# Kernel tuning notes

Hardware: AMD Instinct MI355X
Metric: run time of the kernel (lower is better)

## Reference

```python
import jax, jax.numpy as jnp
import numpy as np

HIDDEN = 1024
HEADS = 16
HEAD_DIM = HIDDEN // HEADS  # 64
MLP_HIDDEN = int(HIDDEN * 4.0)  # 4096
B, L = 2, 2048
EPS_LN = 1e-6
EPS_RMS = 1e-6


def setup_inputs() -> dict:
    key = jax.random.key(0)
    ks = jax.random.split(key, 12)
    s = 0.02
    return {
        "x": jax.random.normal(ks[0], (B, L, HIDDEN), jnp.float32),
        "vec": jax.random.normal(ks[1], (B, HIDDEN), jnp.float32),
        "pe": jax.random.normal(ks[2], (1, 1, L, HEAD_DIM // 2, 2, 2), jnp.float32),
        "w_mod": jax.random.normal(ks[3], (HIDDEN, 3 * HIDDEN), jnp.float32) * s,
        "b_mod": jnp.zeros((3 * HIDDEN,), jnp.float32),
        "w1": jax.random.normal(ks[4], (HIDDEN, 3 * HIDDEN + MLP_HIDDEN), jnp.float32) * s,
        "b1": jnp.zeros((3 * HIDDEN + MLP_HIDDEN,), jnp.float32),
        "w_mlp": jax.random.normal(ks[5], (MLP_HIDDEN, HIDDEN), jnp.float32) * s,
        "b_mlp": jnp.zeros((HIDDEN,), jnp.float32),
        "w2": jax.random.normal(ks[6], (2 * HIDDEN, HIDDEN), jnp.float32) * s,
        "b2": jnp.zeros((HIDDEN,), jnp.float32),
        "q_scale": jnp.ones((HEAD_DIM,), jnp.float32),
        "k_scale": jnp.ones((HEAD_DIM,), jnp.float32),
    }


def _layernorm(x, eps=EPS_LN):
    m = jnp.mean(x, axis=-1, keepdims=True)
    v = jnp.mean(jnp.square(x - m), axis=-1, keepdims=True)
    return (x - m) * jax.lax.rsqrt(v + eps)


def _rmsnorm(x, scale, eps=EPS_RMS):
    rrms = jax.lax.rsqrt(jnp.mean(jnp.square(x), axis=-1, keepdims=True) + eps)
    return x * rrms * scale


def _apply_rope(t, pe):
    # t: [B,H,L,D]; pe: [1,1,L,D//2,2,2]
    t_ = t.reshape(*t.shape[:-1], -1, 1, 2)  # [B,H,L,D//2,1,2]
    out = pe[..., 0] * t_[..., 0] + pe[..., 1] * t_[..., 1]  # [B,H,L,D//2,2]
    return out.reshape(t.shape)


def reference(x, vec, pe, w_mod, b_mod, w1, b1, w_mlp, b_mlp, w2, b2, q_scale, k_scale):
    # adaLN modulation: silu(vec) -> Dense(3*dim) -> shift, scale, gate
    mod = (jax.nn.silu(vec) @ w_mod + b_mod)[:, None, :]  # [B,1,3H]
    shift, scale, gate = jnp.split(mod, 3, axis=-1)
    x_mod = (1.0 + scale) * _layernorm(x) + shift
    # fused QKV + MLP projection
    h = x_mod @ w1 + b1  # [B,L,3H+MH]
    qkv, mlp = h[..., : 3 * HIDDEN], h[..., 3 * HIDDEN :]
    qkv = qkv.reshape(x.shape[0], x.shape[1], 3, HEADS, HEAD_DIM)
    qkv = jnp.transpose(qkv, (2, 0, 3, 1, 4))  # [3,B,H,L,D]
    q, k, v = qkv[0], qkv[1], qkv[2]
    # QK-RMSNorm per head-dim
    q = _rmsnorm(q, q_scale)
    k = _rmsnorm(k, k_scale)
    # RoPE
    q = _apply_rope(q, pe)
    k = _apply_rope(k, pe)
    # attention
    scores = jnp.einsum("bhqd,bhkd->bhqk", q, k) * (HEAD_DIM ** -0.5)
    probs = jax.nn.softmax(scores, axis=-1)
    attn = jnp.einsum("bhqk,bhkd->bhqd", probs, v)
    attn = jnp.transpose(attn, (0, 2, 1, 3)).reshape(x.shape[0], x.shape[1], HIDDEN)
    # mlp branch (Dense with tanh activation per source) + fused output proj
    mlp_out = jnp.tanh(mlp @ w_mlp + b_mlp)
    out = jnp.concatenate([attn, mlp_out], axis=-1) @ w2 + b2
    return x + gate * out
```

## Files before the change

### kernel.cpp

```cpp
#include <hip/hip_runtime.h>
#include <stdint.h>


#define HID  1024
#define NH   16
#define HD   64
#define MLP  4096
#define D1   7168
#define DQKV 3072
#define DCAT 2048
#define BB   2
#define LL   2048
#define TOK  4096

typedef __attribute__((ext_vector_type(8))) short    bf16x8;
typedef __attribute__((ext_vector_type(4))) float    f32x4;
typedef __attribute__((ext_vector_type(4))) unsigned int u32x4;

__device__ __forceinline__ float b2f(unsigned short u) {
    unsigned int v = ((unsigned int)u) << 16;
    float f; __builtin_memcpy(&f, &v, 4); return f;
}
__device__ __forceinline__ unsigned short f2b(float f) {
    unsigned int v; __builtin_memcpy(&v, &f, 4);
    unsigned int r = (v + 0x7FFFu + ((v >> 16) & 1u)) >> 16;
    return (unsigned short)r;
}
__device__ __forceinline__ unsigned int pkbf2(float a, float b) {
    unsigned int ua, ub;
    __builtin_memcpy(&ua, &a, 4); __builtin_memcpy(&ub, &b, 4);
    return ((ua + 0x8000u) >> 16) | ((ub + 0x8000u) & 0xFFFF0000u);
}
__device__ __forceinline__ void gl_lds16(const unsigned short* g, unsigned short* l) {
    __builtin_amdgcn_global_load_lds(
        (const __attribute__((address_space(1))) unsigned int*)(g),
        (__attribute__((address_space(3))) unsigned int*)(l), 16, 0, 0);
}

__global__ void k_transpose_cvt(const float* __restrict__ in,
                                unsigned short* __restrict__ out, int R, int C) {
    __shared__ float tile[32][33];
    int bx = blockIdx.x, by = blockIdx.y;
    int tx = threadIdx.x, ty = threadIdx.y;
    #pragma unroll
    for (int i = 0; i < 4; i++) {
        int r = by * 32 + ty + i * 8;
        int c = bx * 32 + tx;
        tile[ty + i * 8][tx] = in[(size_t)r * C + c];
    }
    __syncthreads();
    #pragma unroll
    for (int i = 0; i < 4; i++) {
        int ro = bx * 32 + ty + i * 8;
        int co = by * 32 + tx;
        out[(size_t)ro * R + co] = f2b(tile[tx][ty + i * 8]);
    }
}

__global__ void k_mod(const float* __restrict__ vec,
                      const float* __restrict__ w_mod,
                      const float* __restrict__ b_mod,
                      float* __restrict__ mod) {
    __shared__ float sv[HID];
    __shared__ float red[8][32];
    int b = blockIdx.y, t = threadIdx.x;
    for (int j = t; j < HID; j += 256) {
        float v = vec[b * HID + j];
        sv[j] = v / (1.0f + __expf(-v));
    }
    __syncthreads();
    int n0 = blockIdx.x * 32;
    int on = t & 31, ks = t >> 5;
    float acc = 0.f;
    const float* wp = w_mod + (size_t)(ks * 128) * 3072 + n0 + on;
    #pragma unroll 4
    for (int k = 0; k < 128; k++) acc += sv[ks * 128 + k] * wp[(size_t)k * 3072];
    red[ks][on] = acc;
    __syncthreads();
    if (t < 32) {
        float s = 0.f;
        #pragma unroll
        for (int i = 0; i < 8; i++) s += red[i][t];
        mod[b * 3072 + n0 + t] = s + b_mod[n0 + t];
    }
}

__global__ void k_lnmod(const float* __restrict__ x,
                        const float* __restrict__ mod,
                        unsigned short* __restrict__ xmod) {
    int tok = blockIdx.x;
    int t = threadIdx.x;
    int b = tok >> 11;
    float4 v4 = *(const float4*)(x + (size_t)tok * HID + t * 4);
    float v0 = v4.x, v1 = v4.y, v2 = v4.z, v3 = v4.w;
    float s  = v0 + v1 + v2 + v3;
    float sq = v0*v0 + v1*v1 + v2*v2 + v3*v3;
    for (int off = 1; off < 64; off <<= 1) {
        s  += __shfl_xor(s,  off);
        sq += __shfl_xor(sq, off);
    }
    __shared__ float ls[4], lq[4];
    int w = t >> 6;
    if ((t & 63) == 0) { ls[w] = s; lq[w] = sq; }
    __syncthreads();
    s  = ls[0] + ls[1] + ls[2] + ls[3];
    sq = lq[0] + lq[1] + lq[2] + lq[3];
    float mean = s * (1.0f / HID);
    float var  = sq * (1.0f / HID) - mean * mean;
    float rstd = rsqrtf(var + 1e-6f);
    const float* mb = mod + b * 3072;
    float y[4] = {v0, v1, v2, v3};
    unsigned short r[4];
    #pragma unroll
    for (int j = 0; j < 4; j++) {
        int col = t * 4 + j;
        float nval = (y[j] - mean) * rstd;
        r[j] = f2b((1.0f + mb[1024 + col]) * nval + mb[col]);
    }
    unsigned int o0 = (unsigned int)r[0] | ((unsigned int)r[1] << 16);
    unsigned int o1 = (unsigned int)r[2] | ((unsigned int)r[3] << 16);
    *(uint2*)(xmod + (size_t)tok * HID + t * 4) = make_uint2(o0, o1);
}

template<int EPI>
__global__ __launch_bounds__(256) void k_gemm(
    const unsigned short* __restrict__ A, int lda,
    const unsigned short* __restrict__ Bt, int ldb,
    const float* __restrict__ bias,
    unsigned short* __restrict__ C, float* __restrict__ Cf, int ldc,
    int K,
    const float* __restrict__ xin,
    const float* __restrict__ mod) {
    __shared__ alignas(16) unsigned short As[128 * 64];
    __shared__ alignas(16) unsigned short Bs[128 * 64];
    int t = threadIdx.x;
    int bm = blockIdx.x, bn = blockIdx.y;
    int lane = t & 63, wave = t >> 6;
    int wm = (wave >> 1) * 64, wn = (wave & 1) * 64;
    int ln = lane & 15, kq = lane >> 4;
    int ln7 = ln & 7;

    f32x4 acc[4][4];
    #pragma unroll
    for (int i = 0; i < 4; i++)
        #pragma unroll
        for (int j = 0; j < 4; j++) acc[i][j] = {0.f, 0.f, 0.f, 0.f};

    int sr  = t >> 3;
    int scg = (t & 7) ^ (sr & 7);
    const unsigned short* Ab = A  + (size_t)(bm * 128) * lda;
    const unsigned short* Bb = Bt + (size_t)(bn * 128) * ldb;

    int ksplit = K / gridDim.z;
    int kbeg = blockIdx.z * ksplit, kend = kbeg + ksplit;

    for (int k0 = kbeg; k0 < kend; k0 += 64) {
        __syncthreads();
        #pragma unroll
        for (int c = 0; c < 4; c++) {
            gl_lds16(Ab + (size_t)(c * 32 + sr) * lda + k0 + scg * 8, &As[c * 2048 + t * 8]);
            gl_lds16(Bb + (size_t)(c * 32 + sr) * ldb + k0 + scg * 8, &Bs[c * 2048 + t * 8]);
        }
        __syncthreads();
        #pragma unroll
        for (int ks = 0; ks < 2; ks++) {
            int slot = ((ks * 4 + kq) ^ ln7) * 8;
            bf16x8 af[4], bfr[4];
            #pragma unroll
            for (int i = 0; i < 4; i++)
                af[i] = *(const bf16x8*)(&As[(wm + i * 16 + ln) * 64 + slot]);
            #pragma unroll
            for (int j = 0; j < 4; j++)
                bfr[j] = *(const bf16x8*)(&Bs[(wn + j * 16 + ln) * 64 + slot]);
            #pragma unroll
            for (int i = 0; i < 4; i++)
                #pragma unroll
                for (int j = 0; j < 4; j++)
                    acc[i][j] = __builtin_amdgcn_mfma_f32_16x16x32_bf16(af[i], bfr[j], acc[i][j], 0, 0, 0);
        }
    }

    #pragma unroll
    for (int i = 0; i < 4; i++) {
        #pragma unroll
        for (int j = 0; j < 4; j++) {
            int col = bn * 128 + wn + j * 16 + ln;
            float bv = (EPI == 3) ? 0.f : bias[col];
            #pragma unroll
            for (int r = 0; r < 4; r++) {
                int row = bm * 128 + wm + i * 16 + kq * 4 + r;
                float v = acc[i][j][r] + bv;
                if (EPI == 0) {
                    C[(size_t)row * ldc + col] = f2b(v);
                } else if (EPI == 1) {
                    C[(size_t)row * ldc + col] = f2b(tanhf(v));
                } else if (EPI == 2) {
                    int b = row >> 11;
                    Cf[(size_t)row * ldc + col] =
                        xin[(size_t)row * HID + col] + mod[b * 3072 + 2048 + col] * v;
                } else {
                    Cf[((size_t)blockIdx.z * TOK + row) * ldc + col] = v;
                }
            }
        }
    }
}

#define KD   1024
#define NT16 16

#define STAGE_A2(BUF, H, KO) do { \
    const unsigned short* s_ = Ab + (size_t)((H) * 128 + sr) * KD + (KO) + scg8; \
    gl_lds16(s_,            &As[BUF][H][t * 8]); \
    gl_lds16(s_ + 64 * KD,  &As[BUF][H][4096 + t * 8]); \
  } while (0)

#define STAGE_B2(BUF, H, KO) do { \
    const unsigned short* s_ = Bb + (size_t)((H) * 128 + sr) * KD + (KO) + scg8; \
    gl_lds16(s_,            &Bs[BUF][H][t * 8]); \
    gl_lds16(s_ + 64 * KD,  &Bs[BUF][H][4096 + t * 8]); \
  } while (0)

#define LDA_H(DST, BUF, MH) do { \
    _Pragma("unroll") \
    for (int i_ = 0; i_ < 4; i_++) { \
      const unsigned short* ap_ = &As[BUF][wmh][(MH) * 4096 + i_ * 1024 + lnx64]; \
      DST[i_][0] = *(const bf16x8*)(ap_ + sA0); \
      DST[i_][1] = *(const bf16x8*)(ap_ + sA1); \
    } \
  } while (0)

#define LDB_H(DST, BUF, NH) do { \
    _Pragma("unroll") \
    for (int j_ = 0; j_ < 2; j_++) { \
      const unsigned short* bp_ = &Bs[BUF][wnh][bro + (NH) * 2048 + j_ * 1024 + lnx64]; \
      DST[j_][0] = *(const bf16x8*)(bp_ + sA0); \
      DST[j_][1] = *(const bf16x8*)(bp_ + sA1); \
    } \
  } while (0)

#define MMQ(AF, BF, IG0, JG0) do { \
    __builtin_amdgcn_s_setprio(1); \
    _Pragma("unroll") \
    for (int ks_ = 0; ks_ < 2; ks_++) \
      _Pragma("unroll") \
      for (int i_ = 0; i_ < 4; i_++) \
        _Pragma("unroll") \
        for (int j_ = 0; j_ < 2; j_++) \
          acc[(IG0) + i_][(JG0) + j_] = __builtin_amdgcn_mfma_f32_16x16x32_bf16( \
              AF[i_][ks_], BF[j_][ks_], acc[(IG0) + i_][(JG0) + j_], 0, 0, 0); \
    __builtin_amdgcn_s_setprio(0); \
  } while (0)

__global__ __launch_bounds__(512, 2) void k_gemm256(
    const unsigned short* __restrict__ A,
    const unsigned short* __restrict__ Bt,
    const float* __restrict__ bias,
    unsigned short* __restrict__ C) {
    __shared__ alignas(16) unsigned short As[2][2][128 * 64];
    __shared__ alignas(16) unsigned short Bs[2][2][128 * 64];

    int wg  = blockIdx.x;
    int cpx = gridDim.x >> 3;
    int swz = (wg & 7) * cpx + (wg >> 3);
    int bm = swz & 15;
    int bn = swz >> 4;

    int t = threadIdx.x;
    int lane = t & 63, wid = t >> 6;
    int wmh = wid >> 2;
    int wnq = wid & 3;
    int wnh = wnq >> 1;
    int bro = (wnq & 1) * 4096;
    int ln = lane & 15, kq = lane >> 4, ln7 = lane & 7;
    int lnx64 = ln * 64;
    int sA0 = ((0 + kq) ^ ln7) * 8;
    int sA1 = ((4 + kq) ^ ln7) * 8;

    int sr   = t >> 3;
    int scg8 = (((t & 7) ^ (sr & 7))) * 8;

    const unsigned short* Ab = A  + (size_t)(bm * 256) * KD;
    const unsigned short* Bb = Bt + (size_t)(bn * 256) * KD;

    f32x4 acc[8][4];
    #pragma unroll
    for (int i = 0; i < 8; i++)
        #pragma unroll
        for (int j = 0; j < 4; j++) acc[i][j] = {0.f, 0.f, 0.f, 0.f};

    STAGE_A2(0, 0, 0);  STAGE_A2(0, 1, 0);
    STAGE_B2(0, 0, 0);  STAGE_B2(0, 1, 0);
    STAGE_A2(1, 0, 64); STAGE_A2(1, 1, 64);
    asm volatile("s_waitcnt vmcnt(4)" ::: "memory");
    __builtin_amdgcn_sched_barrier(0);
    __builtin_amdgcn_s_barrier();

    bf16x8 afA[4][2], afB[4][2], bf0[2][2], bf1[2][2];

    for (int tau = 0; tau < NT16; ++tau) {
        const int q  = tau & 1;
        const int k0 = tau << 6;
        LDA_H(afA, q, 0);
        LDB_H(bf0, q, 0);
        if (tau + 1 < NT16) STAGE_B2(q ^ 1, 0, k0 + 64);
        __builtin_amdgcn_s_barrier();
        asm volatile("s_waitcnt lgkmcnt(0)" ::: "memory");
        __builtin_amdgcn_sched_barrier(0);
        MMQ(afA, bf0, 0, 0);
        __builtin_amdgcn_s_barrier();
        LDA_H(afB, q, 1);
        LDB_H(bf1, q, 1);
        if (tau + 1 < NT16) STAGE_B2(q ^ 1, 1, k0 + 64);
        __builtin_amdgcn_s_barrier();
        asm volatile("s_waitcnt lgkmcnt(0)" ::: "memory");
        __builtin_amdgcn_sched_barrier(0);
        MMQ(afA, bf1, 0, 2);
        __builtin_amdgcn_s_barrier();
        if (tau + 2 < NT16) STAGE_A2(q, 0, k0 + 128);
        MMQ(afB, bf1, 4, 2);
        __builtin_amdgcn_s_barrier();
        if (tau + 2 < NT16) STAGE_A2(q, 1, k0 + 128);
        MMQ(afB, bf0, 4, 0);
        if (tau + 2 < NT16) {
            asm volatile("s_waitcnt vmcnt(4)" ::: "memory");
        } else if (tau + 1 < NT16) {
            asm volatile("s_waitcnt vmcnt(0)" ::: "memory");
        }
        __builtin_amdgcn_sched_barrier(0);
        __builtin_amdgcn_s_barrier();
    }

    #pragma unroll
    for (int jg = 0; jg < 4; jg++) {
        int col = bn * 256 + wnq * 64 + jg * 16 + ln;
        float bv = bias[col];
        #pragma unroll
        for (int ig = 0; ig < 8; ig++) {
            int row = bm * 256 + wmh * 128 + ig * 16 + kq * 4;
            #pragma unroll
            for (int r = 0; r < 4; r++)
                C[(size_t)(row + r) * D1 + col] = f2b(acc[ig][jg][r] + bv);
        }
    }
}

__global__ __launch_bounds__(256) void k_red1(const float* __restrict__ part,
                                              const float* __restrict__ bias,
                                              unsigned short* __restrict__ cat) {
    int idx = blockIdx.x * 256 + threadIdx.x;
    int row = idx >> 8;
    int c4  = (idx & 255) * 4;
    float4 p0 = *(const float4*)(part + (size_t)row * HID + c4);
    float4 p1 = *(const float4*)(part + ((size_t)TOK + row) * HID + c4);
    float4 bv = *(const float4*)(bias + c4);
    float a0 = tanhf(p0.x + p1.x + bv.x);
    float a1 = tanhf(p0.y + p1.y + bv.y);
    float a2 = tanhf(p0.z + p1.z + bv.z);
    float a3 = tanhf(p0.w + p1.w + bv.w);
    *(uint2*)(&cat[(size_t)row * DCAT + HID + c4]) =
        make_uint2(pkbf2(a0, a1), pkbf2(a2, a3));
}

__global__ __launch_bounds__(256) void k_red2(const float* __restrict__ part,
                                              const float* __restrict__ bias,
                                              const float* __restrict__ x,
                                              const float* __restrict__ mod,
                                              float* __restrict__ out) {
    int idx = blockIdx.x * 256 + threadIdx.x;
    int row = idx >> 8;
    int c4  = (idx & 255) * 4;
    int b = row >> 11;
    float4 p0 = *(const float4*)(part + (size_t)row * HID + c4);
    float4 p1 = *(const float4*)(part + ((size_t)TOK + row) * HID + c4);
    float4 bv = *(const float4*)(bias + c4);
    float4 gv = *(const float4*)(mod + b * 3072 + 2048 + c4);
    float4 xv = *(const float4*)(x + (size_t)row * HID + c4);
    float4 o;
    o.x = xv.x + gv.x * (p0.x + p1.x + bv.x);
    o.y = xv.y + gv.y * (p0.y + p1.y + bv.y);
    o.z = xv.z + gv.z * (p0.z + p1.z + bv.z);
    o.w = xv.w + gv.w * (p0.w + p1.w + bv.w);
    *(float4*)(out + (size_t)row * HID + c4) = o;
}

__global__ void k_qkrope(unsigned short* __restrict__ h,
                         const float* __restrict__ pe,
                         const float* __restrict__ q_scale,
                         const float* __restrict__ k_scale) {
    int tok = blockIdx.x;
    int l = tok & (LL - 1);
    int t = threadIdx.x;
    int lane = t & 63, wave = t >> 6;
    int hh = wave * 4 + (lane >> 4);
    int d0 = (lane & 15) * 4;
    unsigned short* row = h + (size_t)tok * D1;
    int i0 = d0 >> 1;
    const float* peb = pe + ((size_t)l * 32 + i0) * 4;
    float4 e0 = *(const float4*)(peb);
    float4 e1 = *(const float4*)(peb + 4);
    #pragma unroll
    for (int qk = 0; qk < 2; qk++) {
        unsigned short* p = row + qk * HID + hh * HD + d0;
        const float* sc = (qk == 0 ? q_scale : k_scale) + d0;
        uint2 qv = *(const uint2*)p;
        float v0 = b2f((unsigned short)(qv.x & 0xFFFF)), v1 = b2f((unsigned short)(qv.x >> 16));
        float v2 = b2f((unsigned short)(qv.y & 0xFFFF)), v3 = b2f((unsigned short)(qv.y >> 16));
        float ssq = v0*v0 + v1*v1 + v2*v2 + v3*v3;
        ssq += __shfl_xor(ssq, 1, 16);
        ssq += __shfl_xor(ssq, 2, 16);
        ssq += __shfl_xor(ssq, 4, 16);
        ssq += __shfl_xor(ssq, 8, 16);
        float rr = rsqrtf(ssq * (1.0f / HD) + 1e-6f);
        if (qk == 0) rr *= 0.18033688011112042f;
        v0 *= rr * sc[0];
        v1 *= rr * sc[1];
        v2 *= rr * sc[2];
        v3 *= rr * sc[3];
        float o0 = e0.x*v0 + e0.y*v1;
        float o1 = e0.z*v0 + e0.w*v1;
        float o2 = e1.x*v2 + e1.y*v3;
        float o3 = e1.z*v2 + e1.w*v3;
        *(uint2*)p = make_uint2(pkbf2(o0, o1), pkbf2(o2, o3));
    }
}

#define KT 64
#define LDP 72
__global__ __launch_bounds__(256) void k_attn(const unsigned short* __restrict__ h,
                                              unsigned short* __restrict__ cat) {
    __shared__ unsigned short Ks[KT * LDP];
    __shared__ unsigned short Vt[HD * LDP];
    __shared__ unsigned short Ps[4 * 16 * LDP];
    int t = threadIdx.x;
    int bx = blockIdx.x;
    int bh = blockIdx.y;
    int b = bh >> 4, hh = bh & 15;
    int lane = t & 63, w = t >> 6;
    int ln = lane & 15, quad = lane >> 4;
    const unsigned short* hb = h + (size_t)b * LL * D1;

    bf16x8 qf[2];
    {
        const unsigned short* qbase = hb + (size_t)(bx * 64 + w * 16) * D1 + hh * HD;
        #pragma unroll
        for (int ks = 0; ks < 2; ks++)
            qf[ks] = *(const bf16x8*)(qbase + (size_t)ln * D1 + ks * 32 + quad * 8);
    }

    f32x4 O[4];
    #pragma unroll
    for (int vn = 0; vn < 4; vn++) O[vn] = {0.f, 0.f, 0.f, 0.f};
    float m_ = -1e30f, l_ = 0.f;

    unsigned short* Psw = Ps + w * 16 * LDP;

    int skey = t >> 2, sdc = (t & 3) * 16;
    int p2 = (t & 31) * 2, db = (t >> 5) * 8;

    for (int kb = 0; kb < LL / KT; kb++) {
        __syncthreads();
        {
            const unsigned short* kbase = hb + (size_t)(kb * KT) * D1 + HID + hh * HD;
            u32x4 ka = *(const u32x4*)(kbase + (size_t)skey * D1 + sdc);
            u32x4 kc = *(const u32x4*)(kbase + (size_t)skey * D1 + sdc + 8);
            *(u32x4*)(&Ks[skey * LDP + sdc]) = ka;
            *(u32x4*)(&Ks[skey * LDP + sdc + 8]) = kc;
            const unsigned short* vbase = hb + (size_t)(kb * KT) * D1 + 2 * HID + hh * HD;
            u32x4 va = *(const u32x4*)(vbase + (size_t)p2 * D1 + db);
            u32x4 vb = *(const u32x4*)(vbase + (size_t)(p2 + 1) * D1 + db);
            #pragma unroll
            for (int j = 0; j < 8; j++) {
                unsigned int lo = (j & 1) ? (va[j >> 1] >> 16) : (va[j >> 1] & 0xFFFFu);
                unsigned int hi = (j & 1) ? (vb[j >> 1] >> 16) : (vb[j >> 1] & 0xFFFFu);
                *(unsigned int*)(&Vt[(db + j) * LDP + p2]) = lo | (hi << 16);
            }
        }
        __syncthreads();

        f32x4 st[4];
        #pragma unroll
        for (int kt = 0; kt < 4; kt++) {
            st[kt] = {0.f, 0.f, 0.f, 0.f};
            #pragma unroll
            for (int ks = 0; ks < 2; ks++) {
                bf16x8 kf = *(const bf16x8*)(&Ks[(kt * 16 + ln) * LDP + ks * 32 + quad * 8]);
                st[kt] = __builtin_amdgcn_mfma_f32_16x16x32_bf16(kf, qf[ks], st[kt], 0, 0, 0);
            }
        }

        {
            float p[16];
            float mx = -1e30f;
            #pragma unroll
            for (int kt = 0; kt < 4; kt++)
                #pragma unroll
                for (int r = 0; r < 4; r++) {
                    float v = st[kt][r];
                    p[kt * 4 + r] = v;
                    mx = fmaxf(mx, v);
                }
            mx = fmaxf(mx, __shfl_xor(mx, 16));
            mx = fmaxf(mx, __shfl_xor(mx, 32));
            float mnew = fmaxf(m_, mx);
            float alpha = __builtin_amdgcn_exp2f(m_ - mnew);
            m_ = mnew;
            float sum = 0.f;
            #pragma unroll
            for (int i = 0; i < 16; i++) {
                float e = __builtin_amdgcn_exp2f(p[i] - mnew);
                p[i] = e;
                sum += e;
            }
            sum += __shfl_xor(sum, 16);
            sum += __shfl_xor(sum, 32);
            l_ = l_ * alpha + sum;
            #pragma unroll
            for (int vn = 0; vn < 4; vn++)
                #pragma unroll
                for (int r = 0; r < 4; r++) O[vn][r] *= alpha;
            #pragma unroll
            for (int kt = 0; kt < 4; kt++) {
                unsigned long long pk =
                    (unsigned long long)pkbf2(p[kt*4+0], p[kt*4+1])
                  | ((unsigned long long)pkbf2(p[kt*4+2], p[kt*4+3]) << 32);
                *(unsigned long long*)(&Psw[ln * LDP + kt * 16 + quad * 4]) = pk;
            }
        }

        #pragma unroll
        for (int kt2 = 0; kt2 < 2; kt2++) {
            bf16x8 pb = *(const bf16x8*)(&Psw[ln * LDP + kt2 * 32 + quad * 8]);
            #pragma unroll
            for (int vn = 0; vn < 4; vn++) {
                bf16x8 vf = *(const bf16x8*)(&Vt[(vn * 16 + ln) * LDP + kt2 * 32 + quad * 8]);
                O[vn] = __builtin_amdgcn_mfma_f32_16x16x32_bf16(vf, pb, O[vn], 0, 0, 0);
            }
        }
    }

    {
        float rl = 1.0f / l_;
        size_t row = (size_t)(b * LL + bx * 64 + w * 16 + ln);
        #pragma unroll
        for (int vn = 0; vn < 4; vn++) {
            #pragma unroll
            for (int r2 = 0; r2 < 4; r2 += 2) {
                unsigned int pk = pkbf2(O[vn][r2] * rl, O[vn][r2 + 1] * rl);
                *(unsigned int*)(&cat[row * DCAT + hh * HD + vn * 16 + quad * 4 + r2]) = pk;
            }
        }
    }
}

extern "C" void kernel_launch(void* const* d_in, const int* in_sizes, int n_in,
                              void* d_out, int out_size, void* d_ws, size_t ws_size,
                              hipStream_t stream) {
    const float* x       = (const float*)d_in[0];
    const float* vec     = (const float*)d_in[1];
    const float* pe      = (const float*)d_in[2];
    const float* w_mod   = (const float*)d_in[3];
    const float* b_mod   = (const float*)d_in[4];
    const float* w1      = (const float*)d_in[5];
    const float* b1      = (const float*)d_in[6];
    const float* w_mlp   = (const float*)d_in[7];
    const float* b_mlp   = (const float*)d_in[8];
    const float* w2      = (const float*)d_in[9];
    const float* b2      = (const float*)d_in[10];
    const float* q_scale = (const float*)d_in[11];
    const float* k_scale = (const float*)d_in[12];
    float* out = (float*)d_out;

    char* ws = (char*)d_ws;
    size_t off = 0;
    float* mod = (float*)(ws + off);                     off += 6144 * 4;
    unsigned short* xmod  = (unsigned short*)(ws + off); off += (size_t)TOK * HID * 2;
    unsigned short* h     = (unsigned short*)(ws + off); off += (size_t)TOK * D1 * 2;
    unsigned short* cat   = (unsigned short*)(ws + off); off += (size_t)TOK * DCAT * 2;
    unsigned short* w1T   = (unsigned short*)(ws + off); off += (size_t)D1 * HID * 2;
    unsigned short* wmlpT = (unsigned short*)(ws + off); off += (size_t)HID * MLP * 2;
    unsigned short* w2T   = (unsigned short*)(ws + off); off += (size_t)HID * DCAT * 2;
    float* part = (float*)(ws + off);                    off += (size_t)2 * TOK * HID * 4;

    k_transpose_cvt<<<dim3(D1 / 32, HID / 32), dim3(32, 8), 0, stream>>>(w1, w1T, HID, D1);
    k_transpose_cvt<<<dim3(HID / 32, MLP / 32), dim3(32, 8), 0, stream>>>(w_mlp, wmlpT, MLP, HID);
    k_transpose_cvt<<<dim3(HID / 32, DCAT / 32), dim3(32, 8), 0, stream>>>(w2, w2T, DCAT, HID);

    k_mod<<<dim3(96, BB), 256, 0, stream>>>(vec, w_mod, b_mod, mod);
    k_lnmod<<<TOK, 256, 0, stream>>>(x, mod, xmod);

    k_gemm256<<<dim3((TOK / 256) * (D1 / 256)), dim3(512), 0, stream>>>(xmod, w1T, b1, h);

    k_qkrope<<<TOK, 256, 0, stream>>>(h, pe, q_scale, k_scale);

    k_attn<<<dim3(LL / 64, BB * NH), 256, 0, stream>>>(h, cat);

    k_gemm<3><<<dim3(TOK / 128, HID / 128, 2), 256, 0, stream>>>(
        h + DQKV, D1, wmlpT, MLP, b_mlp, nullptr, part, HID, MLP, nullptr, nullptr);
    k_red1<<<TOK * HID / 1024, 256, 0, stream>>>(part, b_mlp, cat);

    k_gemm<3><<<dim3(TOK / 128, HID / 128, 2), 256, 0, stream>>>(
        cat, DCAT, w2T, DCAT, b2, nullptr, part, HID, DCAT, nullptr, nullptr);
    k_red2<<<TOK * HID / 1024, 256, 0, stream>>>(part, b2, x, mod, out);
}
```

Measured before the change: 415.1 us.

## Merge weight transposes, reorder GEMM pipeline, and optimize attention loop

Merges the three weight transpose launches into a single kernel. Reorders the main GEMM's LDS staging and MFMA quadrant schedule so B halves load on a different cadence. In attention, it replaces padded LDS with XOR-swizzled layouts, prefetches the next K/V tile into registers, raises wave priority around the MFMAs, and converts with the hardware bf16 pack instruction. It also skips the online-softmax rescale unless the running max grows by more than a threshold. The lazy rescale and the new vmcnt/lgkmcnt waits carry correctness risk if the threshold or counts are wrong.

```diff
diff --git a/kernel.cpp b/kernel.cpp
--- a/kernel.cpp
+++ b/kernel.cpp
@@ -31,16 +31,30 @@
     __builtin_memcpy(&ua, &a, 4); __builtin_memcpy(&ub, &b, 4);
     return ((ua + 0x8000u) >> 16) | ((ub + 0x8000u) & 0xFFFF0000u);
 }
+__device__ __forceinline__ unsigned int cvtpk(float a, float b) {
+    unsigned int r;
+    asm("v_cvt_pk_bf16_f32 %0, %1, %2" : "=v"(r) : "v"(a), "v"(b));
+    return r;
+}
 __device__ __forceinline__ void gl_lds16(const unsigned short* g, unsigned short* l) {
     __builtin_amdgcn_global_load_lds(
         (const __attribute__((address_space(1))) unsigned int*)(g),
         (__attribute__((address_space(3))) unsigned int*)(l), 16, 0, 0);
 }
 
-__global__ void k_transpose_cvt(const float* __restrict__ in,
-                                unsigned short* __restrict__ out, int R, int C) {
+__global__ void k_transpose3(const float* __restrict__ w1, unsigned short* __restrict__ w1T,
+                             const float* __restrict__ wmlp, unsigned short* __restrict__ wmlpT,
+                             const float* __restrict__ w2, unsigned short* __restrict__ w2T) {
     __shared__ float tile[32][33];
-    int bx = blockIdx.x, by = blockIdx.y;
+    int id = blockIdx.x;
+    const float* in; unsigned short* out; int R, C, bx, by;
+    if (id < 7168) {
+        in = w1; out = w1T; R = 1024; C = 7168; bx = id % 224; by = id / 224;
+    } else if (id < 11264) {
+        int j = id - 7168; in = wmlp; out = wmlpT; R = 4096; C = 1024; bx = j & 31; by = j >> 5;
+    } else {
+        int j = id - 11264; in = w2; out = w2T; R = 2048; C = 1024; bx = j & 31; by = j >> 5;
+    }
     int tx = threadIdx.x, ty = threadIdx.y;
     #pragma unroll
     for (int i = 0; i < 4; i++) {
@@ -209,31 +223,31 @@
 #define KD   1024
 #define NT16 16
 
-#define STAGE_A2(BUF, H, KO) do { \
+#define STAGE_A1(BUF, H, KO) do { \
     const unsigned short* s_ = Ab + (size_t)((H) * 128 + sr) * KD + (KO) + scg8; \
-    gl_lds16(s_,            &As[BUF][H][t * 8]); \
-    gl_lds16(s_ + 64 * KD,  &As[BUF][H][4096 + t * 8]); \
+    gl_lds16(s_,           &As[BUF][H][t * 8]); \
+    gl_lds16(s_ + 64 * KD, &As[BUF][H][4096 + t * 8]); \
   } while (0)
 
-#define STAGE_B2(BUF, H, KO) do { \
+#define STAGE_B1(BUF, H, KO) do { \
     const unsigned short* s_ = Bb + (size_t)((H) * 128 + sr) * KD + (KO) + scg8; \
-    gl_lds16(s_,            &Bs[BUF][H][t * 8]); \
-    gl_lds16(s_ + 64 * KD,  &Bs[BUF][H][4096 + t * 8]); \
+    gl_lds16(s_,           &Bs[BUF][H][t * 8]); \
+    gl_lds16(s_ + 64 * KD, &Bs[BUF][H][4096 + t * 8]); \
   } while (0)
 
-#define LDA_H(DST, BUF, MH) do { \
+#define LDA_G(DST, BUF, G) do { \
     _Pragma("unroll") \
     for (int i_ = 0; i_ < 4; i_++) { \
-      const unsigned short* ap_ = &As[BUF][wmh][(MH) * 4096 + i_ * 1024 + lnx64]; \
+      const unsigned short* ap_ = &As[BUF][wmh][(G) * 4096 + i_ * 1024 + lnx64]; \
       DST[i_][0] = *(const bf16x8*)(ap_ + sA0); \
       DST[i_][1] = *(const bf16x8*)(ap_ + sA1); \
     } \
   } while (0)
 
-#define LDB_H(DST, BUF, NH) do { \
+#define LDB_G(DST, BUF, G) do { \
     _Pragma("unroll") \
     for (int j_ = 0; j_ < 2; j_++) { \
-      const unsigned short* bp_ = &Bs[BUF][wnh][bro + (NH) * 2048 + j_ * 1024 + lnx64]; \
+      const unsigned short* bp_ = &Bs[BUF][wnh][bro + (G) * 2048 + j_ * 1024 + lnx64]; \
       DST[j_][0] = *(const bf16x8*)(bp_ + sA0); \
       DST[j_][1] = *(const bf16x8*)(bp_ + sA1); \
     } \
@@ -289,45 +303,48 @@
         #pragma unroll
         for (int j = 0; j < 4; j++) acc[i][j] = {0.f, 0.f, 0.f, 0.f};
 
-    STAGE_A2(0, 0, 0);  STAGE_A2(0, 1, 0);
-    STAGE_B2(0, 0, 0);  STAGE_B2(0, 1, 0);
-    STAGE_A2(1, 0, 64); STAGE_A2(1, 1, 64);
+    STAGE_A1(0, 0, 0);  STAGE_A1(0, 1, 0);
+    STAGE_B1(0, 0, 0);  STAGE_B1(0, 1, 0);
     asm volatile("s_waitcnt vmcnt(4)" ::: "memory");
-    __builtin_amdgcn_sched_barrier(0);
+    STAGE_A1(1, 0, 64); STAGE_A1(1, 1, 64);
+    STAGE_B1(1, 0, 64);
+    asm volatile("s_waitcnt vmcnt(6)" ::: "memory");
     __builtin_amdgcn_s_barrier();
 
-    bf16x8 afA[4][2], afB[4][2], bf0[2][2], bf1[2][2];
+    bf16x8 a0[4][2], a1[4][2], b0[2][2], b1[2][2];
 
     for (int tau = 0; tau < NT16; ++tau) {
         const int q  = tau & 1;
         const int k0 = tau << 6;
-        LDA_H(afA, q, 0);
-        LDB_H(bf0, q, 0);
-        if (tau + 1 < NT16) STAGE_B2(q ^ 1, 0, k0 + 64);
+        LDA_G(a0, q, 0);
+        LDB_G(b0, q, 0);
+        if (tau + 1 < NT16) STAGE_B1(q ^ 1, 1, k0 + 64);
+        asm volatile("s_waitcnt lgkmcnt(8)" ::: "memory");
         __builtin_amdgcn_s_barrier();
         asm volatile("s_waitcnt lgkmcnt(0)" ::: "memory");
         __builtin_amdgcn_sched_barrier(0);
-        MMQ(afA, bf0, 0, 0);
+        MMQ(a0, b0, 0, 0);
         __builtin_amdgcn_s_barrier();
-        LDA_H(afB, q, 1);
-        LDB_H(bf1, q, 1);
-        if (tau + 1 < NT16) STAGE_B2(q ^ 1, 1, k0 + 64);
+        LDA_G(a1, q, 1);
         __builtin_amdgcn_s_barrier();
         asm volatile("s_waitcnt lgkmcnt(0)" ::: "memory");
         __builtin_amdgcn_sched_barrier(0);
-        MMQ(afA, bf1, 0, 2);
+        MMQ(a1, b0, 4, 0);
         __builtin_amdgcn_s_barrier();
-        if (tau + 2 < NT16) STAGE_A2(q, 0, k0 + 128);
-        MMQ(afB, bf1, 4, 2);
+        LDB_G(b1, q, 1);
+        if (tau + 2 < NT16) STAGE_A1(q, 0, k0 + 128);
         __builtin_amdgcn_s_barrier();
-        if (tau + 2 < NT16) STAGE_A2(q, 1, k0 + 128);
-        MMQ(afB, bf0, 4, 0);
+        asm volatile("s_waitcnt lgkmcnt(0)" ::: "memory");
+        __builtin_amdgcn_sched_barrier(0);
+        MMQ(a0, b1, 0, 2);
+        __builtin_amdgcn_s_barrier();
+        if (tau + 2 < NT16) { STAGE_A1(q, 1, k0 + 128); STAGE_B1(q, 0, k0 + 128); }
+        MMQ(a1, b1, 4, 2);
         if (tau + 2 < NT16) {
-            asm volatile("s_waitcnt vmcnt(4)" ::: "memory");
+            asm volatile("s_waitcnt vmcnt(6)" ::: "memory");
         } else if (tau + 1 < NT16) {
             asm volatile("s_waitcnt vmcnt(0)" ::: "memory");
         }
-        __builtin_amdgcn_sched_barrier(0);
         __builtin_amdgcn_s_barrier();
     }
 
@@ -426,19 +443,23 @@
 }
 
 #define KT 64
-#define LDP 72
 __global__ __launch_bounds__(256) void k_attn(const unsigned short* __restrict__ h,
                                               unsigned short* __restrict__ cat) {
-    __shared__ unsigned short Ks[KT * LDP];
-    __shared__ unsigned short Vt[HD * LDP];
-    __shared__ unsigned short Ps[4 * 16 * LDP];
+    __shared__ unsigned short Ks[KT * 64];
+    __shared__ unsigned short Vt[HD * 64];
+    __shared__ unsigned short Ps[4 * 16 * 64];
     int t = threadIdx.x;
     int bx = blockIdx.x;
     int bh = blockIdx.y;
     int b = bh >> 4, hh = bh & 15;
     int lane = t & 63, w = t >> 6;
     int ln = lane & 15, quad = lane >> 4;
+    int ln7 = ln & 7;
     const unsigned short* hb = h + (size_t)b * LL * D1;
+
+    int swk[2];
+    swk[0] = ((0 + quad) ^ ln7) * 8;
+    swk[1] = ((4 + quad) ^ ln7) * 8;
 
     bf16x8 qf[2];
     {
@@ -453,90 +474,109 @@
     for (int vn = 0; vn < 4; vn++) O[vn] = {0.f, 0.f, 0.f, 0.f};
     float m_ = -1e30f, l_ = 0.f;
 
-    unsigned short* Psw = Ps + w * 16 * LDP;
-
-    int skey = t >> 2, sdc = (t & 3) * 16;
+    unsigned short* Psw = Ps + w * 16 * 64;
+
+    int skey = t >> 2, sdc16 = (t & 3) * 16, sc2 = (t & 3) * 2;
     int p2 = (t & 31) * 2, db = (t >> 5) * 8;
+    const unsigned short* kbase0 = hb + HID + hh * HD;
+    const unsigned short* vbase0 = hb + 2 * HID + hh * HD;
+
+    u32x4 ka = *(const u32x4*)(kbase0 + (size_t)skey * D1 + sdc16);
+    u32x4 kc = *(const u32x4*)(kbase0 + (size_t)skey * D1 + sdc16 + 8);
+    u32x4 va = *(const u32x4*)(vbase0 + (size_t)p2 * D1 + db);
+    u32x4 vb = *(const u32x4*)(vbase0 + (size_t)(p2 + 1) * D1 + db);
 
     for (int kb = 0; kb < LL / KT; kb++) {
         __syncthreads();
         {
-            const unsigned short* kbase = hb + (size_t)(kb * KT) * D1 + HID + hh * HD;
-            u32x4 ka = *(const u32x4*)(kbase + (size_t)skey * D1 + sdc);
-            u32x4 kc = *(const u32x4*)(kbase + (size_t)skey * D1 + sdc + 8);
-            *(u32x4*)(&Ks[skey * LDP + sdc]) = ka;
-            *(u32x4*)(&Ks[skey * LDP + sdc + 8]) = kc;
-            const unsigned short* vbase = hb + (size_t)(kb * KT) * D1 + 2 * HID + hh * HD;
-            u32x4 va = *(const u32x4*)(vbase + (size_t)p2 * D1 + db);
-            u32x4 vb = *(const u32x4*)(vbase + (size_t)(p2 + 1) * D1 + db);
+            int k7 = skey & 7;
+            *(u32x4*)(&Ks[skey * 64 + ((sc2 ^ k7) * 8)]) = ka;
+            *(u32x4*)(&Ks[skey * 64 + (((sc2 + 1) ^ k7) * 8)]) = kc;
             #pragma unroll
             for (int j = 0; j < 8; j++) {
                 unsigned int lo = (j & 1) ? (va[j >> 1] >> 16) : (va[j >> 1] & 0xFFFFu);
                 unsigned int hi = (j & 1) ? (vb[j >> 1] >> 16) : (vb[j >> 1] & 0xFFFFu);
-                *(unsigned int*)(&Vt[(db + j) * LDP + p2]) = lo | (hi << 16);
+                int row = db + j;
+                *(unsigned int*)(&Vt[row * 64 + (p2 ^ ((row & 7) << 3))]) = lo | (hi << 16);
             }
         }
         __syncthreads();
+        if (kb + 1 < LL / KT) {
+            const unsigned short* kb1 = kbase0 + (size_t)(kb + 1) * KT * D1;
+            const unsigned short* vb1 = vbase0 + (size_t)(kb + 1) * KT * D1;
+            ka = *(const u32x4*)(kb1 + (size_t)skey * D1 + sdc16);
+            kc = *(const u32x4*)(kb1 + (size_t)skey * D1 + sdc16 + 8);
+            va = *(const u32x4*)(vb1 + (size_t)p2 * D1 + db);
+            vb = *(const u32x4*)(vb1 + (size_t)(p2 + 1) * D1 + db);
+        }
 
         f32x4 st[4];
+        __builtin_amdgcn_s_setprio(1);
         #pragma unroll
         for (int kt = 0; kt < 4; kt++) {
             st[kt] = {0.f, 0.f, 0.f, 0.f};
             #pragma unroll
             for (int ks = 0; ks < 2; ks++) {
-                bf16x8 kf = *(const bf16x8*)(&Ks[(kt * 16 + ln) * LDP + ks * 32 + quad * 8]);
+                bf16x8 kf = *(const bf16x8*)(&Ks[(kt * 16 + ln) * 64 + swk[ks]]);
                 st[kt] = __builtin_amdgcn_mfma_f32_16x16x32_bf16(kf, qf[ks], st[kt], 0, 0, 0);
             }
         }
+        __builtin_amdgcn_s_setprio(0);
 
         {
             float p[16];
-            float mx = -1e30f;
             #pragma unroll
             for (int kt = 0; kt < 4; kt++)
                 #pragma unroll
-                for (int r = 0; r < 4; r++) {
-                    float v = st[kt][r];
-                    p[kt * 4 + r] = v;
-                    mx = fmaxf(mx, v);
-                }
+                for (int r = 0; r < 4; r++) p[kt * 4 + r] = st[kt][r];
+            float a0 = fmaxf(fmaxf(p[0],  p[1]),  p[2]);
+            float a1 = fmaxf(fmaxf(p[3],  p[4]),  p[5]);
+            float a2 = fmaxf(fmaxf(p[6],  p[7]),  p[8]);
+            float a3 = fmaxf(fmaxf(p[9],  p[10]), p[11]);
+            float a4 = fmaxf(fmaxf(p[12], p[13]), p[14]);
+            float mx = fmaxf(fmaxf(fmaxf(a0, a1), a2), fmaxf(fmaxf(a3, a4), p[15]));
             mx = fmaxf(mx, __shfl_xor(mx, 16));
             mx = fmaxf(mx, __shfl_xor(mx, 32));
-            float mnew = fmaxf(m_, mx);
-            float alpha = __builtin_amdgcn_exp2f(m_ - mnew);
-            m_ = mnew;
-            float sum = 0.f;
-            #pragma unroll
-            for (int i = 0; i < 16; i++) {
-                float e = __builtin_amdgcn_exp2f(p[i] - mnew);
-                p[i] = e;
-                sum += e;
+            if (!__all(mx - m_ <= 10.f)) {
+                float mnew = fmaxf(m_, mx);
+                float alpha = __builtin_amdgcn_exp2f(m_ - mnew);
+                m_ = mnew;
+                l_ *= alpha;
+                #pragma unroll
+                for (int vn = 0; vn < 4; vn++)
+                    #pragma unroll
+                    for (int r = 0; r < 4; r++) O[vn][r] *= alpha;
             }
+            #pragma unroll
+            for (int i = 0; i < 16; i++) p[i] = __builtin_amdgcn_exp2f(p[i] - m_);
+            float s0 = (p[0] + p[1]) + (p[2] + p[3]);
+            float s1 = (p[4] + p[5]) + (p[6] + p[7]);
+            float s2 = (p[8] + p[9]) + (p[10] + p[11]);
+            float s3 = (p[12] + p[13]) + (p[14] + p[15]);
+            float sum = (s0 + s1) + (s2 + s3);
             sum += __shfl_xor(sum, 16);
             sum += __shfl_xor(sum, 32);
-            l_ = l_ * alpha + sum;
-            #pragma unroll
-            for (int vn = 0; vn < 4; vn++)
-                #pragma unroll
-                for (int r = 0; r < 4; r++) O[vn][r] *= alpha;
+            l_ += sum;
             #pragma unroll
             for (int kt = 0; kt < 4; kt++) {
-                unsigned long long pk =
-                    (unsigned long long)pkbf2(p[kt*4+0], p[kt*4+1])
-                  | ((unsigned long long)pkbf2(p[kt*4+2], p[kt*4+3]) << 32);
-                *(unsigned long long*)(&Psw[ln * LDP + kt * 16 + quad * 4]) = pk;
+                unsigned int w0 = cvtpk(p[kt*4+0], p[kt*4+1]);
+                unsigned int w1 = cvtpk(p[kt*4+2], p[kt*4+3]);
+                int pchunk = (2 * kt + (quad >> 1)) ^ ln7;
+                *(uint2*)(&Psw[ln * 64 + pchunk * 8 + (quad & 1) * 4]) = make_uint2(w0, w1);
             }
         }
 
+        __builtin_amdgcn_s_setprio(1);
         #pragma unroll
         for (int kt2 = 0; kt2 < 2; kt2++) {
-            bf16x8 pb = *(const bf16x8*)(&Psw[ln * LDP + kt2 * 32 + quad * 8]);
+            bf16x8 pb = *(const bf16x8*)(&Psw[ln * 64 + swk[kt2]]);
             #pragma unroll
             for (int vn = 0; vn < 4; vn++) {
-                bf16x8 vf = *(const bf16x8*)(&Vt[(vn * 16 + ln) * LDP + kt2 * 32 + quad * 8]);
+                bf16x8 vf = *(const bf16x8*)(&Vt[(vn * 16 + ln) * 64 + swk[kt2]]);
                 O[vn] = __builtin_amdgcn_mfma_f32_16x16x32_bf16(vf, pb, O[vn], 0, 0, 0);
             }
         }
+        __builtin_amdgcn_s_setprio(0);
     }
 
     {
@@ -546,7 +586,7 @@
         for (int vn = 0; vn < 4; vn++) {
             #pragma unroll
             for (int r2 = 0; r2 < 4; r2 += 2) {
-                unsigned int pk = pkbf2(O[vn][r2] * rl, O[vn][r2 + 1] * rl);
+                unsigned int pk = cvtpk(O[vn][r2] * rl, O[vn][r2 + 1] * rl);
                 *(unsigned int*)(&cat[row * DCAT + hh * HD + vn * 16 + quad * 4 + r2]) = pk;
             }
         }
@@ -582,9 +622,7 @@
     unsigned short* w2T   = (unsigned short*)(ws + off); off += (size_t)HID * DCAT * 2;
     float* part = (float*)(ws + off);                    off += (size_t)2 * TOK * HID * 4;
 
-    k_transpose_cvt<<<dim3(D1 / 32, HID / 32), dim3(32, 8), 0, stream>>>(w1, w1T, HID, D1);
-    k_transpose_cvt<<<dim3(HID / 32, MLP / 32), dim3(32, 8), 0, stream>>>(w_mlp, wmlpT, MLP, HID);
-    k_transpose_cvt<<<dim3(HID / 32, DCAT / 32), dim3(32, 8), 0, stream>>>(w2, w2T, DCAT, HID);
+    k_transpose3<<<dim3(13312), dim3(32, 8), 0, stream>>>(w1, w1T, w_mlp, wmlpT, w2, w2T);
 
     k_mod<<<dim3(96, BB), 256, 0, stream>>>(vec, w_mod, b_mod, mod);
     k_lnmod<<<TOK, 256, 0, stream>>>(x, mod, xmod);
```

Measured after the change: 397.6 us. -4.2%, faster.
